# Kernel tuning notes

Hardware: AMD Instinct MI355X
Metric: run time of the kernel (lower is better)

The kernel has to match this reference:

```python
import jax, jax.numpy as jnp
import numpy as np

C_CURV = 0.01   # manifold curvature c
EPS = 1e-7
KH = KW = 3
PAD = 1
STRIDE = 1


def log0(y):
    # Poincare-ball log map at origin: artanh(sqrt(c)||y||) * y / (sqrt(c)||y||)
    sqc = jnp.sqrt(jnp.asarray(C_CURV, y.dtype))
    n = jnp.maximum(jnp.linalg.norm(y, axis=-1, keepdims=True), EPS)
    return jnp.arctanh(jnp.clip(sqc * n, 0.0, 1.0 - 1e-6)) * y / (sqc * n)


def exp0(v):
    # Poincare-ball exp map at origin: tanh(sqrt(c)||v||) * v / (sqrt(c)||v||)
    sqc = jnp.sqrt(jnp.asarray(C_CURV, v.dtype))
    n = jnp.maximum(jnp.linalg.norm(v, axis=-1, keepdims=True), EPS)
    return jnp.tanh(sqc * n) * v / (sqc * n)


def setup_inputs() -> dict:
    key = jax.random.key(0)
    k1, k2, k3 = jax.random.split(key, 3)
    x = jax.random.uniform(k1, (4, 32, 256, 256), dtype=jnp.float32)  # points in ball (c=0.01 -> radius 10)
    Wk = jax.random.normal(k2, (KH * KW, 32, 32), dtype=jnp.float32) * 0.05  # [K, C_out, C_in]
    bias = jax.random.normal(k3, (32,), dtype=jnp.float32) * 0.01
    return {"x": x, "Wk": Wk, "bias": bias}


def reference(x, Wk, bias):
    B, Cin, H, W = x.shape
    Hout = (H + 2 * PAD - KH) // STRIDE + 1
    Wout = (W + 2 * PAD - KW) // STRIDE + 1
    xp = jnp.pad(x, ((0, 0), (0, 0), (PAD, PAD), (PAD, PAD)))
    # unfold: one slice per kernel position (i,j), matching F.unfold's (C_in, K, L) layout
    patches = jnp.stack(
        [xp[:, :, i:i + Hout * STRIDE:STRIDE, j:j + Wout * STRIDE:STRIDE]
         for i in range(KH) for j in range(KW)], axis=0)      # [K, B, Cin, Hout, Wout]
    u = log0(jnp.moveaxis(patches, 2, -1))                    # [K, B, Hout, Wout, Cin] tangent vectors
    # PVFC (mobius matvec = exp0(W @ log0(x))) followed by log0 cancels the exp0:
    # log0(PVFC_k(x)) = W_k @ log0(x). Aggregate (sum over k) fused into the einsum.
    v = jnp.einsum('kbhwc,koc->bhwo', u, Wk)                  # [B, Hout, Wout, Cout]
    v = jax.nn.relu(v + bias)
    out = exp0(v)                                             # back to manifold
    return jnp.transpose(out, (0, 3, 1, 2))                   # [B, Cout, Hout, Wout]
```

## Files before the change

### kernel.cpp

```cpp
#include <hip/hip_runtime.h>
#include <math.h>


#define TW 32
#define TH 8
#define HW_ 34
#define NPIX 340
#define CIN 32
#define COUT 32

typedef __attribute__((ext_vector_type(8))) short bf16x8;
typedef __attribute__((ext_vector_type(4))) float f32x4;

__device__ inline unsigned short f2bf(float f) {
    unsigned int u = __builtin_bit_cast(unsigned int, f);
    return (unsigned short)((u + 0x7FFFu + ((u >> 16) & 1u)) >> 16);
}
__device__ inline unsigned int pk2(float a, float b) {
    return (unsigned int)f2bf(a) | ((unsigned int)f2bf(b) << 16);
}

__global__ __launch_bounds__(256) void wprep_kernel(
    const float* __restrict__ Wk, unsigned short* __restrict__ wsW)
{
    int i = blockIdx.x * 256 + threadIdx.x;
    if (i < 9 * 32 * 32) wsW[i] = f2bf(Wk[i]);
}

__global__ __launch_bounds__(512, 8) void pvconv_kernel(
    const float* __restrict__ x, const unsigned short* __restrict__ wsW,
    const float* __restrict__ bias, float* __restrict__ out)
{
    __shared__ __align__(16) unsigned char smem[NPIX * 64];
    unsigned char* u8 = smem;

    const int t  = threadIdx.x;
    const int x0 = blockIdx.x * TW, y0 = blockIdx.y * TH, b = blockIdx.z;

    if (t < 400) {
        const int hy = t / 40, rem = t - hy * 40, j = rem >> 2, cq = rem & 3;
        const int gy = y0 - 1 + hy;
        const int gxb = x0 - 4 + 4 * j;
        const bool ok = ((unsigned)gy < 256u) && !(j == 0 && x0 == 0)
                                              && !(j == 9 && x0 == 224);
        float vv[4][8];
        if (ok) {
            const float* xp = x + (size_t)(b * CIN + cq * 8) * 65536 + gy * 256 + gxb;
            #pragma unroll
            for (int cc = 0; cc < 8; ++cc) {
                float4 f4 = *(const float4*)(xp + (size_t)cc * 65536);
                vv[0][cc] = f4.x; vv[1][cc] = f4.y; vv[2][cc] = f4.z; vv[3][cc] = f4.w;
            }
        } else {
            #pragma unroll
            for (int i = 0; i < 4; ++i)
                #pragma unroll
                for (int cc = 0; cc < 8; ++cc) vv[i][cc] = 0.f;
        }
        float s4[4];
        #pragma unroll
        for (int i = 0; i < 4; ++i) {
            float ss = 0.f;
            #pragma unroll
            for (int cc = 0; cc < 8; ++cc) ss = fmaf(vv[i][cc], vv[i][cc], ss);
            ss += __shfl_xor(ss, 1);
            ss += __shfl_xor(ss, 2);
            float n = fmaxf(sqrtf(ss), 1e-7f);
            float z = fminf(0.1f * n, 1.f - 1e-6f);
            float at = 0.5f * __logf((1.f + z) / (1.f - z));
            s4[i] = at / (0.1f * n);
        }
        const int i0 = (j == 0) ? 3 : 0, i1 = (j == 9) ? 0 : 3;
        #pragma unroll
        for (int i = 0; i < 4; ++i) {
            if (i < i0 || i > i1) continue;
            int p = hy * 34 + 4 * j - 3 + i;
            unsigned int pkk[4];
            #pragma unroll
            for (int w = 0; w < 4; ++w)
                pkk[w] = pk2(vv[i][2 * w] * s4[i], vv[i][2 * w + 1] * s4[i]);
            *(uint4*)(u8 + p * 64 + ((cq ^ ((p >> 1) & 3)) << 4)) = *(uint4*)pkk;
        }
    }
    __syncthreads();

    const int wv = t >> 6, lane = t & 63, m = lane & 15, quad = lane >> 4;
    const float bia0 = bias[m], bia1 = bias[16 + m];

    f32x4 acc[2][2];
    #pragma unroll
    for (int n = 0; n < 2; ++n)
        #pragma unroll
        for (int mt = 0; mt < 2; ++mt) acc[n][mt] = (f32x4)0.f;

    const int pb0 = wv * 34 + m;
    #pragma unroll
    for (int tap = 0; tap < 9; ++tap) {
        const int dy = tap / 3, dx = tap - dy * 3;
        const unsigned short* wrow = wsW + (tap * 32 + m) * 32 + quad * 8;
        bf16x8 B0 = *(const bf16x8*)wrow;
        bf16x8 B1 = *(const bf16x8*)(wrow + 512);
        #pragma unroll
        for (int mt = 0; mt < 2; ++mt) {
            int p = pb0 + mt * 16 + dy * 34 + dx;
            bf16x8 A = *(const bf16x8*)(u8 + p * 64 + ((quad ^ ((p >> 1) & 3)) << 4));
            acc[0][mt] = __builtin_amdgcn_mfma_f32_16x16x32_bf16(A, B0, acc[0][mt], 0, 0, 0);
            acc[1][mt] = __builtin_amdgcn_mfma_f32_16x16x32_bf16(A, B1, acc[1][mt], 0, 0, 0);
        }
    }
    __syncthreads();

    unsigned short* vb = (unsigned short*)smem;
    #pragma unroll
    for (int n = 0; n < 2; ++n)
        #pragma unroll
        for (int mt = 0; mt < 2; ++mt)
            #pragma unroll
            for (int r = 0; r < 4; ++r) {
                int P = wv * 32 + mt * 16 + quad * 4 + r;
                float val = acc[n][mt][r] + (n ? bia1 : bia0);
                vb[P * 40 + n * 16 + m] = f2bf(fmaxf(val, 0.f));
            }
    __syncthreads();

    {
        const int pix = t >> 1, h = t & 1;
        const unsigned short* vp = (const unsigned short*)smem + pix * 40 + h * 16;
        uint4 q0 = *(const uint4*)vp;
        uint4 q1 = *(const uint4*)(vp + 8);
        unsigned int wds[8] = {q0.x, q0.y, q0.z, q0.w, q1.x, q1.y, q1.z, q1.w};
        float qf[16];
        #pragma unroll
        for (int k = 0; k < 8; ++k) {
            qf[2 * k]     = __builtin_bit_cast(float, wds[k] << 16);
            qf[2 * k + 1] = __builtin_bit_cast(float, wds[k] & 0xFFFF0000u);
        }
        float ss = 0.f;
        #pragma unroll
        for (int k = 0; k < 16; ++k) ss = fmaf(qf[k], qf[k], ss);
        ss += __shfl_xor(ss, 1);
        float n = fmaxf(sqrtf(ss), 1e-7f);
        float a = 0.1f * n;
        float e = __expf(-2.f * a);
        float s = (1.f - e) / ((1.f + e) * a);
        const int py = pix >> 5, px = pix & 31;
        const size_t base = (size_t)b * COUT * 65536 + (size_t)(y0 + py) * 256 + (x0 + px);
        #pragma unroll
        for (int cc = 0; cc < 16; ++cc)
            out[base + (size_t)(h * 16 + cc) * 65536] = s * qf[cc];
    }
}

extern "C" void kernel_launch(void* const* d_in, const int* in_sizes, int n_in,
                              void* d_out, int out_size, void* d_ws, size_t ws_size,
                              hipStream_t stream) {
    const float* x    = (const float*)d_in[0];
    const float* Wk   = (const float*)d_in[1];
    const float* bias = (const float*)d_in[2];
    float* out = (float*)d_out;
    unsigned short* wsW = (unsigned short*)d_ws;

    wprep_kernel<<<dim3(36), dim3(256), 0, stream>>>(Wk, wsW);
    dim3 grid(256 / TW, 256 / TH, 4);
    pvconv_kernel<<<grid, dim3(512), 0, stream>>>(x, wsW, bias, out);
}
```

Before: 101.4 us.

## Split log0 into separate pass writing bf16 NHWC tangent buffer, conv reads global

```diff
diff --git a/kernel.cpp b/kernel.cpp
--- a/kernel.cpp
+++ b/kernel.cpp
@@ -4,8 +4,6 @@
 
 #define TW 32
 #define TH 8
-#define HW_ 34
-#define NPIX 340
 #define CIN 32
 #define COUT 32
 
@@ -20,134 +18,119 @@
     return (unsigned int)f2bf(a) | ((unsigned int)f2bf(b) << 16);
 }
 
-__global__ __launch_bounds__(256) void wprep_kernel(
-    const float* __restrict__ Wk, unsigned short* __restrict__ wsW)
+__global__ __launch_bounds__(256) void log0_kernel(
+    const float* __restrict__ x, const float* __restrict__ Wk,
+    unsigned short* __restrict__ wsW, unsigned short* __restrict__ u)
 {
-    int i = blockIdx.x * 256 + threadIdx.x;
-    if (i < 9 * 32 * 32) wsW[i] = f2bf(Wk[i]);
+    const int t = threadIdx.x;
+    const int x0 = blockIdx.x * TW, y0 = blockIdx.y * TH, b = blockIdx.z;
+
+    if (blockIdx.x == 0 && blockIdx.y == 0 && blockIdx.z == 0) {
+        for (int e = t; e < 9 * 32 * 32; e += 256) wsW[e] = f2bf(Wk[e]);
+    }
+
+    const int cq = t & 3, j = (t >> 2) & 7, row = t >> 5;
+    const int gy = y0 + row, gxb = x0 + 4 * j;
+
+    const float* xp = x + (size_t)(b * CIN + cq * 8) * 65536 + gy * 256 + gxb;
+    float vv[4][8];
+    #pragma unroll
+    for (int cc = 0; cc < 8; ++cc) {
+        float4 f4 = *(const float4*)(xp + (size_t)cc * 65536);
+        vv[0][cc] = f4.x; vv[1][cc] = f4.y; vv[2][cc] = f4.z; vv[3][cc] = f4.w;
+    }
+
+    const size_t ubase = ((size_t)b * 65536 + (size_t)gy * 256 + gxb) * 32 + cq * 8;
+    #pragma unroll
+    for (int i = 0; i < 4; ++i) {
+        float ss = 0.f;
+        #pragma unroll
+        for (int cc = 0; cc < 8; ++cc) ss = fmaf(vv[i][cc], vv[i][cc], ss);
+        ss += __shfl_xor(ss, 1);
+        ss += __shfl_xor(ss, 2);
+        float n = fmaxf(sqrtf(ss), 1e-7f);
+        float z = fminf(0.1f * n, 1.f - 1e-6f);
+        float at = 0.5f * __logf((1.f + z) / (1.f - z));
+        float s = at / (0.1f * n);
+        unsigned int pk[4];
+        #pragma unroll
+        for (int w = 0; w < 4; ++w)
+            pk[w] = pk2(vv[i][2 * w] * s, vv[i][2 * w + 1] * s);
+        *(uint4*)(u + ubase + (size_t)i * 32) = *(uint4*)pk;
+    }
 }
 
-__global__ __launch_bounds__(512, 8) void pvconv_kernel(
-    const float* __restrict__ x, const unsigned short* __restrict__ wsW,
+__global__ __launch_bounds__(256) void conv_kernel(
+    const unsigned short* __restrict__ u, const unsigned short* __restrict__ wsW,
     const float* __restrict__ bias, float* __restrict__ out)
 {
-    __shared__ __align__(16) unsigned char smem[NPIX * 64];
-    unsigned char* u8 = smem;
+    __shared__ __align__(16) float v[256 * 36];
 
-    const int t  = threadIdx.x;
+    const int t = threadIdx.x;
     const int x0 = blockIdx.x * TW, y0 = blockIdx.y * TH, b = blockIdx.z;
+    const int wv = t >> 6, lane = t & 63, m = lane & 15, quad = lane >> 4;
 
-    if (t < 400) {
-        const int hy = t / 40, rem = t - hy * 40, j = rem >> 2, cq = rem & 3;
-        const int gy = y0 - 1 + hy;
-        const int gxb = x0 - 4 + 4 * j;
-        const bool ok = ((unsigned)gy < 256u) && !(j == 0 && x0 == 0)
-                                              && !(j == 9 && x0 == 224);
-        float vv[4][8];
-        if (ok) {
-            const float* xp = x + (size_t)(b * CIN + cq * 8) * 65536 + gy * 256 + gxb;
-            #pragma unroll
-            for (int cc = 0; cc < 8; ++cc) {
-                float4 f4 = *(const float4*)(xp + (size_t)cc * 65536);
-                vv[0][cc] = f4.x; vv[1][cc] = f4.y; vv[2][cc] = f4.z; vv[3][cc] = f4.w;
-            }
-        } else {
-            #pragma unroll
-            for (int i = 0; i < 4; ++i)
-                #pragma unroll
-                for (int cc = 0; cc < 8; ++cc) vv[i][cc] = 0.f;
-        }
-        float s4[4];
-        #pragma unroll
-        for (int i = 0; i < 4; ++i) {
-            float ss = 0.f;
-            #pragma unroll
-            for (int cc = 0; cc < 8; ++cc) ss = fmaf(vv[i][cc], vv[i][cc], ss);
-            ss += __shfl_xor(ss, 1);
-            ss += __shfl_xor(ss, 2);
-            float n = fmaxf(sqrtf(ss), 1e-7f);
-            float z = fminf(0.1f * n, 1.f - 1e-6f);
-            float at = 0.5f * __logf((1.f + z) / (1.f - z));
-            s4[i] = at / (0.1f * n);
-        }
-        const int i0 = (j == 0) ? 3 : 0, i1 = (j == 9) ? 0 : 3;
-        #pragma unroll
-        for (int i = 0; i < 4; ++i) {
-            if (i < i0 || i > i1) continue;
-            int p = hy * 34 + 4 * j - 3 + i;
-            unsigned int pkk[4];
-            #pragma unroll
-            for (int w = 0; w < 4; ++w)
-                pkk[w] = pk2(vv[i][2 * w] * s4[i], vv[i][2 * w + 1] * s4[i]);
-            *(uint4*)(u8 + p * 64 + ((cq ^ ((p >> 1) & 3)) << 4)) = *(uint4*)pkk;
-        }
-    }
-    __syncthreads();
-
-    const int wv = t >> 6, lane = t & 63, m = lane & 15, quad = lane >> 4;
-    const float bia0 = bias[m], bia1 = bias[16 + m];
-
-    f32x4 acc[2][2];
+    f32x4 acc[2][4];
     #pragma unroll
     for (int n = 0; n < 2; ++n)
         #pragma unroll
-        for (int mt = 0; mt < 2; ++mt) acc[n][mt] = (f32x4)0.f;
+        for (int mt = 0; mt < 4; ++mt) acc[n][mt] = (f32x4)0.f;
 
-    const int pb0 = wv * 34 + m;
+    const size_t bb = (size_t)b * 65536;
     #pragma unroll
     for (int tap = 0; tap < 9; ++tap) {
-        const int dy = tap / 3, dx = tap - dy * 3;
+        const int dy = tap / 3, dx = tap - 3 * dy;
         const unsigned short* wrow = wsW + (tap * 32 + m) * 32 + quad * 8;
         bf16x8 B0 = *(const bf16x8*)wrow;
         bf16x8 B1 = *(const bf16x8*)(wrow + 512);
         #pragma unroll
-        for (int mt = 0; mt < 2; ++mt) {
-            int p = pb0 + mt * 16 + dy * 34 + dx;
-            bf16x8 A = *(const bf16x8*)(u8 + p * 64 + ((quad ^ ((p >> 1) & 3)) << 4));
+        for (int mt = 0; mt < 4; ++mt) {
+            const int pb = wv * 64 + mt * 16;
+            const int gy = y0 + (pb >> 5) + dy - 1;
+            const int gx = x0 + (pb & 31) + m + dx - 1;
+            bf16x8 A;
+            #pragma unroll
+            for (int e = 0; e < 8; ++e) A[e] = 0;
+            if ((unsigned)gy < 256u && (unsigned)gx < 256u)
+                A = *(const bf16x8*)(u + (bb + (size_t)gy * 256 + gx) * 32 + quad * 8);
             acc[0][mt] = __builtin_amdgcn_mfma_f32_16x16x32_bf16(A, B0, acc[0][mt], 0, 0, 0);
             acc[1][mt] = __builtin_amdgcn_mfma_f32_16x16x32_bf16(A, B1, acc[1][mt], 0, 0, 0);
         }
     }
-    __syncthreads();
 
-    unsigned short* vb = (unsigned short*)smem;
+    const float bia0 = bias[m], bia1 = bias[16 + m];
     #pragma unroll
     for (int n = 0; n < 2; ++n)
         #pragma unroll
-        for (int mt = 0; mt < 2; ++mt)
+        for (int mt = 0; mt < 4; ++mt)
             #pragma unroll
             for (int r = 0; r < 4; ++r) {
-                int P = wv * 32 + mt * 16 + quad * 4 + r;
+                int pix = wv * 64 + mt * 16 + quad * 4 + r;
                 float val = acc[n][mt][r] + (n ? bia1 : bia0);
-                vb[P * 40 + n * 16 + m] = f2bf(fmaxf(val, 0.f));
+                v[pix * 36 + n * 16 + m] = fmaxf(val, 0.f);
             }
     __syncthreads();
 
     {
-        const int pix = t >> 1, h = t & 1;
-        const unsigned short* vp = (const unsigned short*)smem + pix * 40 + h * 16;
-        uint4 q0 = *(const uint4*)vp;
-        uint4 q1 = *(const uint4*)(vp + 8);
-        unsigned int wds[8] = {q0.x, q0.y, q0.z, q0.w, q1.x, q1.y, q1.z, q1.w};
-        float qf[16];
+        float q[COUT];
+        const float4* vp = (const float4*)&v[t * 36];
         #pragma unroll
-        for (int k = 0; k < 8; ++k) {
-            qf[2 * k]     = __builtin_bit_cast(float, wds[k] << 16);
-            qf[2 * k + 1] = __builtin_bit_cast(float, wds[k] & 0xFFFF0000u);
+        for (int jj = 0; jj < 8; ++jj) {
+            float4 c4 = vp[jj];
+            q[4 * jj] = c4.x; q[4 * jj + 1] = c4.y; q[4 * jj + 2] = c4.z; q[4 * jj + 3] = c4.w;
         }
         float ss = 0.f;
         #pragma unroll
-        for (int k = 0; k < 16; ++k) ss = fmaf(qf[k], qf[k], ss);
-        ss += __shfl_xor(ss, 1);
+        for (int o = 0; o < COUT; ++o) ss = fmaf(q[o], q[o], ss);
         float n = fmaxf(sqrtf(ss), 1e-7f);
         float a = 0.1f * n;
         float e = __expf(-2.f * a);
         float s = (1.f - e) / ((1.f + e) * a);
-        const int py = pix >> 5, px = pix & 31;
+        const int px = t & 31, py = t >> 5;
         const size_t base = (size_t)b * COUT * 65536 + (size_t)(y0 + py) * 256 + (x0 + px);
         #pragma unroll
-        for (int cc = 0; cc < 16; ++cc)
-            out[base + (size_t)(h * 16 + cc) * 65536] = s * qf[cc];
+        for (int o = 0; o < COUT; ++o)
+            out[base + (size_t)o * 65536] = s * q[o];
     }
 }
 
@@ -158,9 +141,11 @@
     const float* Wk   = (const float*)d_in[1];
     const float* bias = (const float*)d_in[2];
     float* out = (float*)d_out;
+
     unsigned short* wsW = (unsigned short*)d_ws;
+    unsigned short* u   = (unsigned short*)((char*)d_ws + 32768);
 
-    wprep_kernel<<<dim3(36), dim3(256), 0, stream>>>(Wk, wsW);
     dim3 grid(256 / TW, 256 / TH, 4);
-    pvconv_kernel<<<grid, dim3(512), 0, stream>>>(x, wsW, bias, out);
+    log0_kernel<<<grid, dim3(256), 0, stream>>>(x, Wk, wsW, u);
+    conv_kernel<<<grid, dim3(256), 0, stream>>>(u, wsW, bias, out);
 }
```

After: 106.6 us. +5.1%, slower.
